# Kernel optimization log

Hardware: AMD Instinct MI355X
Metric: run time of the kernel (lower is better)

Reference implementation:

```python
import jax, jax.numpy as jnp
import numpy as np

B, N, C = 2, 384, 11            # images, proposals/img, classes (incl background)
RCN = 5                          # (xc, yc, w, h, angle_deg)
WEIGHTS = (10.0, 10.0, 5.0, 5.0, 1.0)
SCORE_THRESH = 0.05
NMS_THRESH = 0.5
DET_PER_IMG = 100
BBOX_XFORM_CLIP = float(np.log(1000.0 / 16.0))
EPS = 1e-8


def setup_inputs() -> dict:
    key = jax.random.key(0)
    k1, k2, k3, k4, k5 = jax.random.split(key, 5)
    class_logits = jax.random.normal(k1, (B * N, C), jnp.float32) * 2.0
    box_regression = jax.random.normal(k2, (B * N, C * RCN), jnp.float32) * 0.5
    xy = jax.random.uniform(k3, (B * N, 2), jnp.float32, 0.0, 1024.0)
    wh = jax.random.uniform(k4, (B * N, 2), jnp.float32, 16.0, 256.0)
    ang = jax.random.uniform(k5, (B * N, 1), jnp.float32, -90.0, 90.0)
    rrects = jnp.concatenate([xy, wh, ang], -1)
    return {"class_logits": class_logits, "box_regression": box_regression, "rrects": rrects}


def cross2(a, b):
    return a[..., 0] * b[..., 1] - a[..., 1] * b[..., 0]


def decode(rel, anchors):
    # rel (...,5) deltas, anchors (...,5) rotated boxes; relative angle coder
    wx, wy, ww, wh, wa = WEIGHTS
    dx = rel[..., 0] / wx
    dy = rel[..., 1] / wy
    dw = jnp.clip(rel[..., 2] / ww, None, BBOX_XFORM_CLIP)
    dh = jnp.clip(rel[..., 3] / wh, None, BBOX_XFORM_CLIP)
    da = rel[..., 4] / wa
    xc, yc, w, h, a = (anchors[..., i] for i in range(5))
    px = dx * w + xc
    py = dy * h + yc
    pw = jnp.exp(dw) * w
    ph = jnp.exp(dh) * h
    pa = da * (180.0 / np.pi) + a
    pa = (pa + 180.0) % 360.0 - 180.0
    return jnp.stack([px, py, pw, ph, pa], -1)


def corners(b):
    # (...,5) -> (...,4,2) rectangle corners (CCW in box frame)
    xc, yc, w, h, a = (b[..., i] for i in range(5))
    t = a * (np.pi / 180.0)
    c, s = jnp.cos(t), jnp.sin(t)
    hx, hy = w * 0.5, h * 0.5
    lx = jnp.stack([-hx, hx, hx, -hx], -1)
    ly = jnp.stack([-hy, -hy, hy, hy], -1)
    px = xc[..., None] + lx * c[..., None] - ly * s[..., None]
    py = yc[..., None] + lx * s[..., None] + ly * c[..., None]
    return jnp.stack([px, py], -1)


def inter_area(ca, cb):
    # intersection area of two convex quads (4,2),(4,2): candidate points =
    # 16 edge-edge intersections + 8 contained corners, sorted by angle, shoelace
    a0, b0 = ca, cb
    d1 = jnp.roll(ca, -1, 0) - ca
    d2 = jnp.roll(cb, -1, 0) - cb
    den = cross2(d1[:, None, :], d2[None, :, :])                # (4,4)
    diff = b0[None, :, :] - a0[:, None, :]
    den_s = jnp.where(jnp.abs(den) < EPS, 1.0, den)
    t = cross2(diff, d2[None, :, :]) / den_s
    u = cross2(diff, d1[:, None, :]) / den_s
    ok = (jnp.abs(den) >= EPS) & (t >= 0) & (t <= 1) & (u >= 0) & (u <= 1)
    pint = a0[:, None, :] + t[..., None] * d1[:, None, :]       # (4,4,2)

    def inside(p, cs):
        ev = jnp.roll(cs, -1, 0) - cs
        cr = cross2(ev[None, :, :], p[:, None, :] - cs[None, :, :])  # (4,4)
        return jnp.all(cr >= -1e-6, -1) | jnp.all(cr <= 1e-6, -1)

    pts = jnp.concatenate([pint.reshape(16, 2), ca, cb], 0)     # (24,2)
    msk = jnp.concatenate([ok.reshape(16), inside(ca, cb), inside(cb, ca)], 0)
    nv = jnp.sum(msk)
    cen = jnp.sum(pts * msk[:, None], 0) / jnp.maximum(nv, 1)
    pts = jnp.where(msk[:, None], pts, cen)                     # park invalid at centroid
    ang = jnp.arctan2(pts[:, 1] - cen[1], pts[:, 0] - cen[0])
    p = pts[jnp.argsort(ang)]
    area = 0.5 * jnp.abs(jnp.sum(cross2(p, jnp.roll(p, -1, 0))))
    return jnp.where(nv >= 3, area, 0.0)


def rotated_iou_matrix(boxes):
    # boxes (N,5) -> (N,N) rotated IoU
    cs = corners(boxes)
    area = boxes[:, 2] * boxes[:, 3]
    inter = jax.vmap(lambda ci: jax.vmap(lambda cj: inter_area(ci, cj))(cs))(cs)
    return inter / (area[:, None] + area[None, :] - inter + EPS)


def greedy_nms(iou, scores, valid):
    n = iou.shape[0]
    order = jnp.argsort(-jnp.where(valid, scores, -jnp.inf))
    ios = iou[order][:, order]
    vs = valid[order]
    idx = jnp.arange(n)

    def body(i, sup):
        cur_ok = (~sup[i]) & vs[i]
        return sup | (cur_ok & (ios[i] > NMS_THRESH) & (idx > i))

    sup = jax.lax.fori_loop(0, n, body, jnp.zeros((n,), bool))
    keep_sorted = (~sup) & vs
    return jnp.zeros((n,), bool).at[order].set(keep_sorted)


def reference(class_logits, box_regression, rrects):
    prob = jax.nn.softmax(class_logits, -1)                     # (M,C)
    rel = box_regression.reshape(B * N, C, RCN)
    dec = decode(rel, rrects[:, None, :])                       # (M,C,5)
    boxes = dec.reshape(B, N, C, RCN)
    scores = prob.reshape(B, N, C)
    fg_boxes = jnp.moveaxis(boxes[:, :, 1:, :], 2, 1)           # (B,C-1,N,5)
    fg_scores = jnp.moveaxis(scores[:, :, 1:], 2, 1)            # (B,C-1,N)
    valid = fg_scores > SCORE_THRESH
    iou = jax.vmap(jax.vmap(rotated_iou_matrix))(fg_boxes)      # (B,C-1,N,N)
    keep = jax.vmap(jax.vmap(greedy_nms))(iou, fg_scores, valid)
    flat_scores = jnp.where(keep, fg_scores, -1.0).reshape(B, (C - 1) * N)
    top_s, top_i = jax.lax.top_k(flat_scores, DET_PER_IMG)
    sel_boxes = jnp.take_along_axis(fg_boxes.reshape(B, (C - 1) * N, RCN), top_i[:, :, None], axis=1)
    labels = top_i // N + 1
    ok = top_s > 0.0
    out = jnp.concatenate([jnp.where(ok[..., None], sel_boxes, 0.0), jnp.where(ok, top_s, 0.0)[..., None]], -1)
    labels = jnp.where(ok, labels, 0)
    return out, labels
```

## Files before the change

kernel.cpp:

```cpp
#include <hip/hip_runtime.h>
#include <cmath>

#define NPROP 384
#define NB 2
#define NCLS 11
#define NFG 10
#define BC_TOTAL (NB*NFG)
#define M_TOTAL (NB*NPROP)
#define FLAT_PER_IMG (NFG*NPROP)
#define DET 100
#define PAIR_SLICE 3072

#define OFF_BOXES 0
#define OFF_AREA  38400
#define OFF_SCORE 46080
#define OFF_SUP   53760
#define OFF_KIDX  145920
#define OFF_KSC   153600
#define OFF_KCNT  161280
#define OFF_PCNT  161312
#define OFF_PAIRS 161344

typedef unsigned long long ull;

__device__ __forceinline__ void mk_corners(float px, float py, float pw, float ph, float pa,
                                           float cxo[4], float cyo[4]) {
    float t = pa * 0.017453292519943295f;
    float ct = cosf(t), st = sinf(t);
    float hx = pw*0.5f, hy = ph*0.5f;
    float lx[4] = {-hx, hx, hx, -hx};
    float ly[4] = {-hy, -hy, hy, hy};
#pragma unroll
    for (int k = 0; k < 4; ++k) {
        cxo[k] = px + lx[k]*ct - ly[k]*st;
        cyo[k] = py + lx[k]*st + ly[k]*ct;
    }
}

__device__ float inter_area_net(const float ax[4], const float ay[4],
                                const float bx[4], const float by[4]) {
    float d1x[4], d1y[4], d2x[4], d2y[4];
#pragma unroll
    for (int k = 0; k < 4; ++k) {
        int k1 = (k + 1) & 3;
        d1x[k] = ax[k1] - ax[k]; d1y[k] = ay[k1] - ay[k];
        d2x[k] = bx[k1] - bx[k]; d2y[k] = by[k1] - by[k];
    }
    float ex[32], ey[32];
    bool msk[24];
#pragma unroll
    for (int i = 0; i < 4; ++i) {
#pragma unroll
        for (int j = 0; j < 4; ++j) {
            float den = d1x[i]*d2y[j] - d1y[i]*d2x[j];
            float dfx = bx[j]-ax[i], dfy = by[j]-ay[i];
            float dens = (fabsf(den) < 1e-8f) ? 1.0f : den;
            float t = (dfx*d2y[j] - dfy*d2x[j]) / dens;
            float u = (dfx*d1y[i] - dfy*d1x[i]) / dens;
            bool ok = (fabsf(den) >= 1e-8f) && t >= 0.0f && t <= 1.0f
                                            && u >= 0.0f && u <= 1.0f;
            ex[i*4+j] = ax[i] + t*d1x[i];
            ey[i*4+j] = ay[i] + t*d1y[i];
            msk[i*4+j] = ok;
        }
    }
#pragma unroll
    for (int i = 0; i < 4; ++i) {
        bool allp = true, alln = true;
#pragma unroll
        for (int j = 0; j < 4; ++j) {
            float cr = d2x[j]*(ay[i]-by[j]) - d2y[j]*(ax[i]-bx[j]);
            allp = allp && (cr >= -1e-6f);
            alln = alln && (cr <= 1e-6f);
        }
        ex[16+i] = ax[i]; ey[16+i] = ay[i]; msk[16+i] = allp || alln;
    }
#pragma unroll
    for (int i = 0; i < 4; ++i) {
        bool allp = true, alln = true;
#pragma unroll
        for (int j = 0; j < 4; ++j) {
            float cr = d1x[j]*(by[i]-ay[j]) - d1y[j]*(bx[i]-ax[j]);
            allp = allp && (cr >= -1e-6f);
            alln = alln && (cr <= 1e-6f);
        }
        ex[20+i] = bx[i]; ey[20+i] = by[i]; msk[20+i] = allp || alln;
    }
    int nv = 0; float sx = 0.f, sy = 0.f;
#pragma unroll
    for (int k = 0; k < 24; ++k)
        if (msk[k]) { nv++; sx += ex[k]; sy += ey[k]; }
    float fm = (float)(nv > 1 ? nv : 1);
    float cx = sx / fm, cy = sy / fm;
    unsigned key[32];
#pragma unroll
    for (int k = 0; k < 24; ++k) {
        float qx = msk[k] ? ex[k] : cx;
        float qy = msk[k] ? ey[k] : cy;
        ex[k] = qx; ey[k] = qy;
        float dx = qx - cx, dy = qy - cy;
        float den = fabsf(dx) + fabsf(dy);
        float r = (den > 0.0f) ? dy / den : 0.0f;
        float p = (dx >= 0.0f) ? r : ((dy >= 0.0f) ? 2.0f - r : -2.0f - r);
        p = p + 0.0f;
        unsigned u = __float_as_uint(p);
        u = (u & 0x80000000u) ? ~u : (u | 0x80000000u);
        key[k] = (u & 0xFFFFFFE0u) | (unsigned)k;
    }
#pragma unroll
    for (int k = 24; k < 32; ++k) { key[k] = 0xFFFFFFFFu; ex[k] = 0.f; ey[k] = 0.f; }
#pragma unroll
    for (int k = 2; k <= 32; k <<= 1) {
#pragma unroll
        for (int j = k >> 1; j > 0; j >>= 1) {
#pragma unroll
            for (int i = 0; i < 32; ++i) {
                int l = i ^ j;
                if (l > i) {
                    bool up = ((i & k) == 0);
                    unsigned ka = key[i], kb = key[l];
                    bool sw = up ? (ka > kb) : (ka < kb);
                    float xa = ex[i], xb = ex[l];
                    float ya = ey[i], yb = ey[l];
                    key[i] = sw ? kb : ka; key[l] = sw ? ka : kb;
                    ex[i]  = sw ? xb : xa; ex[l]  = sw ? xa : xb;
                    ey[i]  = sw ? yb : ya; ey[l]  = sw ? ya : yb;
                }
            }
        }
    }
    float s = 0.f;
#pragma unroll
    for (int k = 0; k < 24; ++k) {
        int n = (k + 1 == 24) ? 0 : (k + 1);
        s += ex[k]*ey[n] - ey[k]*ex[n];
    }
    float area = 0.5f * fabsf(s);
    return (nv >= 3) ? area : 0.0f;
}

__device__ __forceinline__ void eval_pair_glob(float* ws, int bc, int hi, int lo) {
    const float* boxes = ws + OFF_BOXES;
    const float* areaA = ws + OFF_AREA;
    unsigned int* supw = (unsigned int*)(ws + OFF_SUP);
    int rowi = bc*NPROP + hi, rowj = bc*NPROP + lo;
    float axp[4], ayp[4], bxp[4], byp[4];
    mk_corners(boxes[rowi*5+0], boxes[rowi*5+1], boxes[rowi*5+2],
               boxes[rowi*5+3], boxes[rowi*5+4], axp, ayp);
    mk_corners(boxes[rowj*5+0], boxes[rowj*5+1], boxes[rowj*5+2],
               boxes[rowj*5+3], boxes[rowj*5+4], bxp, byp);
    float inter = inter_area_net(axp, ayp, bxp, byp);
    float iou = inter / (areaA[rowi] + areaA[rowj] - inter + 1e-8f);
    if (iou > 0.5f)
        atomicOr(&supw[rowi*12 + (lo >> 5)], 1u << (lo & 31));
}

__global__ __launch_bounds__(384)
void pairgen_kernel(const float* __restrict__ logits,
                    const float* __restrict__ boxreg,
                    const float* __restrict__ rrects,
                    float* __restrict__ ws,
                    float* __restrict__ out) {
    __shared__ float pxL[NPROP], pyL[NPROP], radL[NPROP], areaL[NPROP], scoreL[NPROP];
    __shared__ int   origL[NPROP];
    __shared__ int   wbase[8];
    __shared__ int   pcntS;
    int bc = blockIdx.x, t = threadIdx.x;
    int b = bc / NFG, cls = (bc % NFG) + 1;
    int wv = t >> 6, lane = t & 63;

    int gq = bc*NPROP + t;
    if (gq < NB*DET*6 + NB*DET) out[gq] = 0.0f;
    if (t == 0) pcntS = 0;
    {
        unsigned int* supw = (unsigned int*)(ws + OFF_SUP) + bc*NPROP*12;
        for (int k = t; k < NPROP*12; k += NPROP) supw[k] = 0u;
    }
    float prob;
    {
        int m = b*NPROP + t;
        float lg[NCLS];
        float mx = -INFINITY;
#pragma unroll
        for (int c = 0; c < NCLS; ++c) { lg[c] = logits[m*NCLS+c]; mx = fmaxf(mx, lg[c]); }
        float sum = 0.f;
#pragma unroll
        for (int c = 0; c < NCLS; ++c) sum += expf(lg[c]-mx);
        prob = expf(lg[cls]-mx) / sum;
        float axc = rrects[m*5+0], ayc = rrects[m*5+1];
        float aw  = rrects[m*5+2], ah  = rrects[m*5+3], aa = rrects[m*5+4];
        const float* rel = boxreg + m*(NCLS*5) + cls*5;
        float dx = rel[0] / 10.0f;
        float dy = rel[1] / 10.0f;
        float dw = fminf(rel[2] / 5.0f, 4.1351665567423205f);
        float dh = fminf(rel[3] / 5.0f, 4.1351665567423205f);
        float da = rel[4];
        float px = dx*aw + axc;
        float py = dy*ah + ayc;
        float pw = expf(dw)*aw;
        float ph = expf(dh)*ah;
        float pa = da*57.29577951308232f + aa;
        float xm = pa + 180.0f;
        float r = fmodf(xm, 360.0f);
        if (r < 0.0f) r += 360.0f;
        pa = r - 180.0f;
        pxL[t]=px; pyL[t]=py; areaL[t]=pw*ph; scoreL[t]=prob;
        radL[t]=0.5f*sqrtf(pw*pw + ph*ph);
        float* boxes = ws + OFF_BOXES;
        int o = bc*NPROP + t;
        boxes[o*5+0]=px; boxes[o*5+1]=py; boxes[o*5+2]=pw; boxes[o*5+3]=ph; boxes[o*5+4]=pa;
        ws[OFF_AREA + o]  = pw*ph;
        ws[OFF_SCORE + o] = prob;
    }
    bool vi = prob > 0.05f;
    ull vb = __ballot(vi);
    if (lane == 0) wbase[wv] = __popcll(vb);
    __syncthreads();
    if (t == 0) {
        int s = 0;
#pragma unroll
        for (int w = 0; w < 6; ++w) { int c = wbase[w]; wbase[w] = s; s += c; }
        wbase[6] = s;
    }
    __syncthreads();
    if (vi) origL[wbase[wv] + (int)__popcll(vb & ((1ull << lane) - 1ull))] = t;
    __syncthreads();
    int cnt = wbase[6];

    unsigned int* pairs = (unsigned int*)(ws + OFF_PAIRS) + bc*PAIR_SLICE;
    for (int a = wv; a < cnt; a += 6) {
        int ia = origL[a];
        float cxa = pxL[ia], cya = pyL[ia], ra = radL[ia], Aa = areaL[ia], sa = scoreL[ia];
        for (int b0 = a + 1; b0 < cnt; b0 += 64) {
            int bb = b0 + lane;
            bool go = false; int ib = 0;
            if (bb < cnt) {
                ib = origL[bb];
                float ddx = cxa - pxL[ib], ddy = cya - pyL[ib];
                float rr = ra + radL[ib];
                go = (ddx*ddx + ddy*ddy <= rr*rr);
                float Ab = areaL[ib];
                float mn = fminf(Aa, Ab);
                go = go && (3.0f*mn > Aa + Ab);
            }
            ull m = __ballot(go);
            int base = 0;
            if (lane == 0 && m) base = atomicAdd(&pcntS, __popcll(m));
            base = __shfl(base, 0);
            if (go) {
                float sb = scoreL[ib];
                bool afirst = (sa > sb) || (sa == sb && ia < ib);
                int hi = afirst ? ia : ib;
                int lo = afirst ? ib : ia;
                int pos = base + (int)__popcll(m & ((1ull << lane) - 1ull));
                if (pos < PAIR_SLICE)
                    pairs[pos] = ((unsigned)hi << 10) | (unsigned)lo;
                else
                    eval_pair_glob(ws, bc, hi, lo);
            }
        }
    }
    __syncthreads();
    if (t == 0) ((unsigned int*)(ws + OFF_PCNT))[bc] = (unsigned)pcntS;
}

__global__ __launch_bounds__(256)
void heavy_kernel(float* __restrict__ ws) {
    int bc = blockIdx.x >> 4;
    int chunk = blockIdx.x & 15;
    unsigned n = ((const unsigned int*)(ws + OFF_PCNT))[bc];
    if (n > PAIR_SLICE) n = PAIR_SLICE;
    const unsigned int* pairs = (const unsigned int*)(ws + OFF_PAIRS) + bc*PAIR_SLICE;
    for (unsigned p = chunk*256u + threadIdx.x; p < n; p += 4096u) {
        unsigned pk = pairs[p];
        eval_pair_glob(ws, bc, (int)(pk >> 10), (int)(pk & 0x3FFu));
    }
}

__global__ __launch_bounds__(384)
void nms_kernel(float* __restrict__ ws) {
    __shared__ ull keyL[NPROP];
    __shared__ int orderL[NPROP];
    __shared__ ull supL[NPROP*6];
    __shared__ unsigned char keepS[NPROP];
    __shared__ int wcntS[8];
    int bc = blockIdx.x, t = threadIdx.x;
    int wv = t >> 6, lane = t & 63;
    const float* scoreA = ws + OFF_SCORE;
    const ull* supG = (const ull*)(ws + OFF_SUP);
    float sc = scoreA[bc*NPROP + t];
    bool vi = sc > 0.05f;
    ull myk = vi ? (((ull)__float_as_uint(sc) << 32) | (ull)(0xFFFFFFFFu - (unsigned)t))
                 : (ull)(0xFFFFFFFFu - (unsigned)t);
    keyL[t] = myk;
    keepS[t] = 0;
    ull vb = __ballot(vi);
    if (lane == 0) wcntS[wv] = __popcll(vb);
    __syncthreads();
    {
        int r = 0;
        for (int k = 0; k < NPROP; k += 8) {
            int acc = 0;
#pragma unroll
            for (int q = 0; q < 8; ++q) acc += (keyL[k+q] > myk) ? 1 : 0;
            r += acc;
        }
        orderL[r] = t;
    }
    for (int k = t; k < NPROP*6; k += NPROP) supL[k] = supG[bc*NPROP*6 + k];
    __syncthreads();
    int NV = wcntS[0] + wcntS[1] + wcntS[2] + wcntS[3] + wcntS[4] + wcntS[5];
    if (t < 64) {
        int ord0 = orderL[lane],      ord1 = orderL[64+lane];
        int ord2 = orderL[128+lane],  ord3 = orderL[192+lane];
        int ord4 = orderL[256+lane],  ord5 = orderL[320+lane];
        ull mask = 0ull;
        int o_cur = __shfl(ord0, 0);
        ull row_cur = (lane < 6) ? supL[o_cur*6 + lane] : 0ull;
        for (int p = 0; p < NV; ++p) {
            int pn = (p + 1 < NPROP) ? (p + 1) : 0;
            int seg = pn >> 6, sl = pn & 63;
            int on = __shfl(ord0, sl);
            on = (seg == 1) ? __shfl(ord1, sl) : on;
            on = (seg == 2) ? __shfl(ord2, sl) : on;
            on = (seg == 3) ? __shfl(ord3, sl) : on;
            on = (seg == 4) ? __shfl(ord4, sl) : on;
            on = (seg == 5) ? __shfl(ord5, sl) : on;
            ull row_next = (lane < 6) ? supL[on*6 + lane] : 0ull;
            bool myhit = (lane == (o_cur >> 6)) && ((mask >> (o_cur & 63)) & 1ull);
            ull bal = __ballot(myhit);
            if (bal == 0ull) {
                if (lane == 0) keepS[o_cur] = 1;
                mask |= row_cur;
            }
            row_cur = row_next;
            o_cur = on;
        }
    }
    __syncthreads();
    bool kp = keepS[t] != 0;
    ull bal = __ballot(kp);
    if (lane == 0) wcntS[wv] = __popcll(bal);
    __syncthreads();
    if (t == 0) {
        int s = 0;
#pragma unroll
        for (int w = 0; w < 6; ++w) { int c = wcntS[w]; wcntS[w] = s; s += c; }
        ((unsigned int*)(ws + OFF_KCNT))[bc] = (unsigned)s;
    }
    __syncthreads();
    if (kp) {
        int pos = wcntS[wv] + (int)__popcll(bal & ((1ull << lane) - 1ull));
        ((unsigned int*)(ws + OFF_KIDX))[bc*NPROP + pos] = (unsigned)((bc % NFG)*NPROP + t);
        (ws + OFF_KSC)[bc*NPROP + pos] = sc;
    }
}

__global__ __launch_bounds__(256)
void topk_kernel(const float* __restrict__ ws, float* __restrict__ out) {
    __shared__ ull keyL[FLAT_PER_IMG];
    int b = blockIdx.x >> 4;
    int slice = blockIdx.x & 15;
    int t = threadIdx.x;
    const unsigned int* kidx2 = (const unsigned int*)(ws + OFF_KIDX);
    const float* ksc2 = ws + OFF_KSC;
    const unsigned int* kcnt2 = (const unsigned int*)(ws + OFF_KCNT);
    const float* boxes = ws + OFF_BOXES;
    int offs[NFG], cnts[NFG];
    int K = 0;
#pragma unroll
    for (int fg = 0; fg < NFG; ++fg) {
        cnts[fg] = (int)kcnt2[b*NFG + fg];
        offs[fg] = K;
        K += cnts[fg];
    }
#pragma unroll
    for (int fg = 0; fg < NFG; ++fg) {
        int bc = b*NFG + fg;
        for (int k = t; k < cnts[fg]; k += 256) {
            unsigned sb = __float_as_uint(ksc2[bc*NPROP + k]);
            unsigned f  = kidx2[bc*NPROP + k];
            keyL[offs[fg] + k] = ((ull)sb << 32) | (ull)(0xFFFFFFFFu - f);
        }
    }
    int KP = (K + 15) & ~15;
    for (int k = K + t; k < KP; k += 256) keyL[k] = 0ull;
    __syncthreads();
    int e = slice*256 + t;
    if (e >= K) return;
    ull my = keyL[e];
    int r = 0;
    for (int k = 0; k < KP; k += 16) {
        int acc = 0;
#pragma unroll
        for (int q = 0; q < 16; ++q)
            acc += (keyL[k+q] > my) ? 1 : 0;
        r += acc;
    }
    if (r < DET) {
        unsigned f = 0xFFFFFFFFu - (unsigned)(my & 0xFFFFFFFFu);
        float s = __uint_as_float((unsigned)(my >> 32));
        int src = b*FLAT_PER_IMG + (int)f;
        float* row = out + (b*DET + r)*6;
#pragma unroll
        for (int q = 0; q < 5; ++q) row[q] = boxes[src*5+q];
        row[5] = s;
        out[NB*DET*6 + b*DET + r] = (float)(f / NPROP + 1);
    }
}

extern "C" void kernel_launch(void* const* d_in, const int* in_sizes, int n_in,
                              void* d_out, int out_size, void* d_ws, size_t ws_size,
                              hipStream_t stream) {
    const float* logits = (const float*)d_in[0];
    const float* boxreg = (const float*)d_in[1];
    const float* rrects = (const float*)d_in[2];
    float* out = (float*)d_out;
    float* ws  = (float*)d_ws;
    (void)in_sizes; (void)n_in; (void)out_size; (void)ws_size;

    pairgen_kernel<<<BC_TOTAL, NPROP, 0, stream>>>(logits, boxreg, rrects, ws, out);
    heavy_kernel<<<BC_TOTAL * 16, 256, 0, stream>>>(ws);
    nms_kernel<<<BC_TOTAL, NPROP, 0, stream>>>(ws);
    topk_kernel<<<NB * 16, 256, 0, stream>>>(ws, out);
}
```

Before: 143.2 us.

## Fuse four NMS stages into one cooperative kernel with grid syncs

Merges the pair-generation, pair-evaluation, NMS and top-k kernels into a single cooperative launch of 160 blocks of 384 threads, separated by grid-wide syncs. Each stage reuses one shared memory buffer. The aim is to remove three kernel launch gaps and their inter-kernel overhead. In exchange it pays grid.sync costs, and the heavy stage and top-k are repartitioned: 8 chunks per class instead of 16, and 10 slices of 384 per image.

After: 191.7 us. 33.9% more time.

```diff
diff --git a/kernel.cpp b/kernel.cpp
--- a/kernel.cpp
+++ b/kernel.cpp
@@ -1,5 +1,8 @@
 #include <hip/hip_runtime.h>
+#include <hip/hip_cooperative_groups.h>
 #include <cmath>
+
+namespace cg = cooperative_groups;
 
 #define NPROP 384
 #define NB 2
@@ -10,6 +13,7 @@
 #define FLAT_PER_IMG (NFG*NPROP)
 #define DET 100
 #define PAIR_SLICE 3072
+#define GRID_BLKS 160
 
 #define OFF_BOXES 0
 #define OFF_AREA  38400
@@ -155,257 +159,265 @@
         atomicOr(&supw[rowi*12 + (lo >> 5)], 1u << (lo & 31));
 }
 
+#define SMEM_BYTES 30720
+
 __global__ __launch_bounds__(384)
-void pairgen_kernel(const float* __restrict__ logits,
-                    const float* __restrict__ boxreg,
-                    const float* __restrict__ rrects,
-                    float* __restrict__ ws,
-                    float* __restrict__ out) {
-    __shared__ float pxL[NPROP], pyL[NPROP], radL[NPROP], areaL[NPROP], scoreL[NPROP];
-    __shared__ int   origL[NPROP];
-    __shared__ int   wbase[8];
-    __shared__ int   pcntS;
-    int bc = blockIdx.x, t = threadIdx.x;
-    int b = bc / NFG, cls = (bc % NFG) + 1;
+void fused_kernel(const float* __restrict__ logits,
+                  const float* __restrict__ boxreg,
+                  const float* __restrict__ rrects,
+                  float* __restrict__ ws,
+                  float* __restrict__ out) {
+    cg::grid_group grid = cg::this_grid();
+    __shared__ __align__(16) unsigned char smemRaw[SMEM_BYTES];
+    __shared__ int auxA[8];
+    __shared__ int auxB;
+    int blk = blockIdx.x, t = threadIdx.x;
     int wv = t >> 6, lane = t & 63;
 
-    int gq = bc*NPROP + t;
-    if (gq < NB*DET*6 + NB*DET) out[gq] = 0.0f;
-    if (t == 0) pcntS = 0;
+    if (blk < BC_TOTAL) {
+        float* pxL    = (float*)smemRaw;
+        float* pyL    = pxL + NPROP;
+        float* radL   = pyL + NPROP;
+        float* areaL  = radL + NPROP;
+        float* scoreL = areaL + NPROP;
+        int*   origL  = (int*)(scoreL + NPROP);
+        int bc = blk;
+        int b = bc / NFG, cls = (bc % NFG) + 1;
+        int gq = bc*NPROP + t;
+        if (gq < NB*DET*6 + NB*DET) out[gq] = 0.0f;
+        if (t == 0) auxB = 0;
+        {
+            unsigned int* supw = (unsigned int*)(ws + OFF_SUP) + bc*NPROP*12;
+            for (int k = t; k < NPROP*12; k += NPROP) supw[k] = 0u;
+        }
+        float prob;
+        {
+            int m = b*NPROP + t;
+            float lg[NCLS];
+            float mx = -INFINITY;
+#pragma unroll
+            for (int c = 0; c < NCLS; ++c) { lg[c] = logits[m*NCLS+c]; mx = fmaxf(mx, lg[c]); }
+            float sum = 0.f;
+#pragma unroll
+            for (int c = 0; c < NCLS; ++c) sum += expf(lg[c]-mx);
+            prob = expf(lg[cls]-mx) / sum;
+            float axc = rrects[m*5+0], ayc = rrects[m*5+1];
+            float aw  = rrects[m*5+2], ah  = rrects[m*5+3], aa = rrects[m*5+4];
+            const float* rel = boxreg + m*(NCLS*5) + cls*5;
+            float dx = rel[0] / 10.0f;
+            float dy = rel[1] / 10.0f;
+            float dw = fminf(rel[2] / 5.0f, 4.1351665567423205f);
+            float dh = fminf(rel[3] / 5.0f, 4.1351665567423205f);
+            float da = rel[4];
+            float px = dx*aw + axc;
+            float py = dy*ah + ayc;
+            float pw = expf(dw)*aw;
+            float ph = expf(dh)*ah;
+            float pa = da*57.29577951308232f + aa;
+            float xm = pa + 180.0f;
+            float r = fmodf(xm, 360.0f);
+            if (r < 0.0f) r += 360.0f;
+            pa = r - 180.0f;
+            pxL[t]=px; pyL[t]=py; areaL[t]=pw*ph; scoreL[t]=prob;
+            radL[t]=0.5f*sqrtf(pw*pw + ph*ph);
+            float* boxes = ws + OFF_BOXES;
+            int o = bc*NPROP + t;
+            boxes[o*5+0]=px; boxes[o*5+1]=py; boxes[o*5+2]=pw; boxes[o*5+3]=ph; boxes[o*5+4]=pa;
+            ws[OFF_AREA + o]  = pw*ph;
+            ws[OFF_SCORE + o] = prob;
+        }
+        bool vi = prob > 0.05f;
+        ull vb = __ballot(vi);
+        if (lane == 0) auxA[wv] = __popcll(vb);
+        __syncthreads();
+        if (t == 0) {
+            int s = 0;
+#pragma unroll
+            for (int w = 0; w < 6; ++w) { int c = auxA[w]; auxA[w] = s; s += c; }
+            auxA[6] = s;
+        }
+        __syncthreads();
+        if (vi) origL[auxA[wv] + (int)__popcll(vb & ((1ull << lane) - 1ull))] = t;
+        __syncthreads();
+        int cnt = auxA[6];
+        unsigned int* pairs = (unsigned int*)(ws + OFF_PAIRS) + bc*PAIR_SLICE;
+        for (int a = wv; a < cnt; a += 6) {
+            int ia = origL[a];
+            float cxa = pxL[ia], cya = pyL[ia], ra = radL[ia], Aa = areaL[ia], sa = scoreL[ia];
+            for (int b0 = a + 1; b0 < cnt; b0 += 64) {
+                int bb = b0 + lane;
+                bool go = false; int ib = 0;
+                if (bb < cnt) {
+                    ib = origL[bb];
+                    float ddx = cxa - pxL[ib], ddy = cya - pyL[ib];
+                    float rr = ra + radL[ib];
+                    go = (ddx*ddx + ddy*ddy <= rr*rr);
+                    float Ab = areaL[ib];
+                    float mn = fminf(Aa, Ab);
+                    go = go && (3.0f*mn > Aa + Ab);
+                }
+                ull m = __ballot(go);
+                int base = 0;
+                if (lane == 0 && m) base = atomicAdd(&auxB, __popcll(m));
+                base = __shfl(base, 0);
+                if (go) {
+                    float sb = scoreL[ib];
+                    bool afirst = (sa > sb) || (sa == sb && ia < ib);
+                    int hi = afirst ? ia : ib;
+                    int lo = afirst ? ib : ia;
+                    int pos = base + (int)__popcll(m & ((1ull << lane) - 1ull));
+                    if (pos < PAIR_SLICE)
+                        pairs[pos] = ((unsigned)hi << 10) | (unsigned)lo;
+                    else
+                        eval_pair_glob(ws, bc, hi, lo);
+                }
+            }
+        }
+        __syncthreads();
+        if (t == 0) ((unsigned int*)(ws + OFF_PCNT))[bc] = (unsigned)auxB;
+    }
+    grid.sync();
+
     {
-        unsigned int* supw = (unsigned int*)(ws + OFF_SUP) + bc*NPROP*12;
-        for (int k = t; k < NPROP*12; k += NPROP) supw[k] = 0u;
-    }
-    float prob;
-    {
-        int m = b*NPROP + t;
-        float lg[NCLS];
-        float mx = -INFINITY;
-#pragma unroll
-        for (int c = 0; c < NCLS; ++c) { lg[c] = logits[m*NCLS+c]; mx = fmaxf(mx, lg[c]); }
-        float sum = 0.f;
-#pragma unroll
-        for (int c = 0; c < NCLS; ++c) sum += expf(lg[c]-mx);
-        prob = expf(lg[cls]-mx) / sum;
-        float axc = rrects[m*5+0], ayc = rrects[m*5+1];
-        float aw  = rrects[m*5+2], ah  = rrects[m*5+3], aa = rrects[m*5+4];
-        const float* rel = boxreg + m*(NCLS*5) + cls*5;
-        float dx = rel[0] / 10.0f;
-        float dy = rel[1] / 10.0f;
-        float dw = fminf(rel[2] / 5.0f, 4.1351665567423205f);
-        float dh = fminf(rel[3] / 5.0f, 4.1351665567423205f);
-        float da = rel[4];
-        float px = dx*aw + axc;
-        float py = dy*ah + ayc;
-        float pw = expf(dw)*aw;
-        float ph = expf(dh)*ah;
-        float pa = da*57.29577951308232f + aa;
-        float xm = pa + 180.0f;
-        float r = fmodf(xm, 360.0f);
-        if (r < 0.0f) r += 360.0f;
-        pa = r - 180.0f;
-        pxL[t]=px; pyL[t]=py; areaL[t]=pw*ph; scoreL[t]=prob;
-        radL[t]=0.5f*sqrtf(pw*pw + ph*ph);
-        float* boxes = ws + OFF_BOXES;
-        int o = bc*NPROP + t;
-        boxes[o*5+0]=px; boxes[o*5+1]=py; boxes[o*5+2]=pw; boxes[o*5+3]=ph; boxes[o*5+4]=pa;
-        ws[OFF_AREA + o]  = pw*ph;
-        ws[OFF_SCORE + o] = prob;
-    }
-    bool vi = prob > 0.05f;
-    ull vb = __ballot(vi);
-    if (lane == 0) wbase[wv] = __popcll(vb);
-    __syncthreads();
-    if (t == 0) {
-        int s = 0;
-#pragma unroll
-        for (int w = 0; w < 6; ++w) { int c = wbase[w]; wbase[w] = s; s += c; }
-        wbase[6] = s;
-    }
-    __syncthreads();
-    if (vi) origL[wbase[wv] + (int)__popcll(vb & ((1ull << lane) - 1ull))] = t;
-    __syncthreads();
-    int cnt = wbase[6];
-
-    unsigned int* pairs = (unsigned int*)(ws + OFF_PAIRS) + bc*PAIR_SLICE;
-    for (int a = wv; a < cnt; a += 6) {
-        int ia = origL[a];
-        float cxa = pxL[ia], cya = pyL[ia], ra = radL[ia], Aa = areaL[ia], sa = scoreL[ia];
-        for (int b0 = a + 1; b0 < cnt; b0 += 64) {
-            int bb = b0 + lane;
-            bool go = false; int ib = 0;
-            if (bb < cnt) {
-                ib = origL[bb];
-                float ddx = cxa - pxL[ib], ddy = cya - pyL[ib];
-                float rr = ra + radL[ib];
-                go = (ddx*ddx + ddy*ddy <= rr*rr);
-                float Ab = areaL[ib];
-                float mn = fminf(Aa, Ab);
-                go = go && (3.0f*mn > Aa + Ab);
-            }
-            ull m = __ballot(go);
-            int base = 0;
-            if (lane == 0 && m) base = atomicAdd(&pcntS, __popcll(m));
-            base = __shfl(base, 0);
-            if (go) {
-                float sb = scoreL[ib];
-                bool afirst = (sa > sb) || (sa == sb && ia < ib);
-                int hi = afirst ? ia : ib;
-                int lo = afirst ? ib : ia;
-                int pos = base + (int)__popcll(m & ((1ull << lane) - 1ull));
-                if (pos < PAIR_SLICE)
-                    pairs[pos] = ((unsigned)hi << 10) | (unsigned)lo;
-                else
-                    eval_pair_glob(ws, bc, hi, lo);
-            }
-        }
-    }
-    __syncthreads();
-    if (t == 0) ((unsigned int*)(ws + OFF_PCNT))[bc] = (unsigned)pcntS;
-}
-
-__global__ __launch_bounds__(256)
-void heavy_kernel(float* __restrict__ ws) {
-    int bc = blockIdx.x >> 4;
-    int chunk = blockIdx.x & 15;
-    unsigned n = ((const unsigned int*)(ws + OFF_PCNT))[bc];
-    if (n > PAIR_SLICE) n = PAIR_SLICE;
-    const unsigned int* pairs = (const unsigned int*)(ws + OFF_PAIRS) + bc*PAIR_SLICE;
-    for (unsigned p = chunk*256u + threadIdx.x; p < n; p += 4096u) {
-        unsigned pk = pairs[p];
-        eval_pair_glob(ws, bc, (int)(pk >> 10), (int)(pk & 0x3FFu));
-    }
-}
-
-__global__ __launch_bounds__(384)
-void nms_kernel(float* __restrict__ ws) {
-    __shared__ ull keyL[NPROP];
-    __shared__ int orderL[NPROP];
-    __shared__ ull supL[NPROP*6];
-    __shared__ unsigned char keepS[NPROP];
-    __shared__ int wcntS[8];
-    int bc = blockIdx.x, t = threadIdx.x;
-    int wv = t >> 6, lane = t & 63;
-    const float* scoreA = ws + OFF_SCORE;
-    const ull* supG = (const ull*)(ws + OFF_SUP);
-    float sc = scoreA[bc*NPROP + t];
-    bool vi = sc > 0.05f;
-    ull myk = vi ? (((ull)__float_as_uint(sc) << 32) | (ull)(0xFFFFFFFFu - (unsigned)t))
-                 : (ull)(0xFFFFFFFFu - (unsigned)t);
-    keyL[t] = myk;
-    keepS[t] = 0;
-    ull vb = __ballot(vi);
-    if (lane == 0) wcntS[wv] = __popcll(vb);
-    __syncthreads();
-    {
-        int r = 0;
-        for (int k = 0; k < NPROP; k += 8) {
-            int acc = 0;
-#pragma unroll
-            for (int q = 0; q < 8; ++q) acc += (keyL[k+q] > myk) ? 1 : 0;
-            r += acc;
-        }
-        orderL[r] = t;
-    }
-    for (int k = t; k < NPROP*6; k += NPROP) supL[k] = supG[bc*NPROP*6 + k];
-    __syncthreads();
-    int NV = wcntS[0] + wcntS[1] + wcntS[2] + wcntS[3] + wcntS[4] + wcntS[5];
-    if (t < 64) {
-        int ord0 = orderL[lane],      ord1 = orderL[64+lane];
-        int ord2 = orderL[128+lane],  ord3 = orderL[192+lane];
-        int ord4 = orderL[256+lane],  ord5 = orderL[320+lane];
-        ull mask = 0ull;
-        int o_cur = __shfl(ord0, 0);
-        ull row_cur = (lane < 6) ? supL[o_cur*6 + lane] : 0ull;
-        for (int p = 0; p < NV; ++p) {
-            int pn = (p + 1 < NPROP) ? (p + 1) : 0;
-            int seg = pn >> 6, sl = pn & 63;
-            int on = __shfl(ord0, sl);
-            on = (seg == 1) ? __shfl(ord1, sl) : on;
-            on = (seg == 2) ? __shfl(ord2, sl) : on;
-            on = (seg == 3) ? __shfl(ord3, sl) : on;
-            on = (seg == 4) ? __shfl(ord4, sl) : on;
-            on = (seg == 5) ? __shfl(ord5, sl) : on;
-            ull row_next = (lane < 6) ? supL[on*6 + lane] : 0ull;
-            bool myhit = (lane == (o_cur >> 6)) && ((mask >> (o_cur & 63)) & 1ull);
-            ull bal = __ballot(myhit);
-            if (bal == 0ull) {
-                if (lane == 0) keepS[o_cur] = 1;
-                mask |= row_cur;
-            }
-            row_cur = row_next;
-            o_cur = on;
-        }
-    }
-    __syncthreads();
-    bool kp = keepS[t] != 0;
-    ull bal = __ballot(kp);
-    if (lane == 0) wcntS[wv] = __popcll(bal);
-    __syncthreads();
-    if (t == 0) {
-        int s = 0;
-#pragma unroll
-        for (int w = 0; w < 6; ++w) { int c = wcntS[w]; wcntS[w] = s; s += c; }
-        ((unsigned int*)(ws + OFF_KCNT))[bc] = (unsigned)s;
-    }
-    __syncthreads();
-    if (kp) {
-        int pos = wcntS[wv] + (int)__popcll(bal & ((1ull << lane) - 1ull));
-        ((unsigned int*)(ws + OFF_KIDX))[bc*NPROP + pos] = (unsigned)((bc % NFG)*NPROP + t);
-        (ws + OFF_KSC)[bc*NPROP + pos] = sc;
-    }
-}
-
-__global__ __launch_bounds__(256)
-void topk_kernel(const float* __restrict__ ws, float* __restrict__ out) {
-    __shared__ ull keyL[FLAT_PER_IMG];
-    int b = blockIdx.x >> 4;
-    int slice = blockIdx.x & 15;
-    int t = threadIdx.x;
-    const unsigned int* kidx2 = (const unsigned int*)(ws + OFF_KIDX);
-    const float* ksc2 = ws + OFF_KSC;
-    const unsigned int* kcnt2 = (const unsigned int*)(ws + OFF_KCNT);
-    const float* boxes = ws + OFF_BOXES;
-    int offs[NFG], cnts[NFG];
-    int K = 0;
-#pragma unroll
-    for (int fg = 0; fg < NFG; ++fg) {
-        cnts[fg] = (int)kcnt2[b*NFG + fg];
-        offs[fg] = K;
-        K += cnts[fg];
-    }
-#pragma unroll
-    for (int fg = 0; fg < NFG; ++fg) {
-        int bc = b*NFG + fg;
-        for (int k = t; k < cnts[fg]; k += 256) {
-            unsigned sb = __float_as_uint(ksc2[bc*NPROP + k]);
-            unsigned f  = kidx2[bc*NPROP + k];
-            keyL[offs[fg] + k] = ((ull)sb << 32) | (ull)(0xFFFFFFFFu - f);
-        }
-    }
-    int KP = (K + 15) & ~15;
-    for (int k = K + t; k < KP; k += 256) keyL[k] = 0ull;
-    __syncthreads();
-    int e = slice*256 + t;
-    if (e >= K) return;
-    ull my = keyL[e];
-    int r = 0;
-    for (int k = 0; k < KP; k += 16) {
-        int acc = 0;
-#pragma unroll
-        for (int q = 0; q < 16; ++q)
-            acc += (keyL[k+q] > my) ? 1 : 0;
-        r += acc;
-    }
-    if (r < DET) {
-        unsigned f = 0xFFFFFFFFu - (unsigned)(my & 0xFFFFFFFFu);
-        float s = __uint_as_float((unsigned)(my >> 32));
-        int src = b*FLAT_PER_IMG + (int)f;
-        float* row = out + (b*DET + r)*6;
-#pragma unroll
-        for (int q = 0; q < 5; ++q) row[q] = boxes[src*5+q];
-        row[5] = s;
-        out[NB*DET*6 + b*DET + r] = (float)(f / NPROP + 1);
+        int bc = blk >> 3;
+        int chunk = blk & 7;
+        unsigned n = ((const unsigned int*)(ws + OFF_PCNT))[bc];
+        if (n > PAIR_SLICE) n = PAIR_SLICE;
+        const unsigned int* pairs = (const unsigned int*)(ws + OFF_PAIRS) + bc*PAIR_SLICE;
+        for (unsigned p = chunk*384u + t; p < n; p += 8u*384u) {
+            unsigned pk = pairs[p];
+            eval_pair_glob(ws, bc, (int)(pk >> 10), (int)(pk & 0x3FFu));
+        }
+    }
+    grid.sync();
+
+    if (blk < BC_TOTAL) {
+        ull* keyL   = (ull*)smemRaw;
+        ull* supL   = (ull*)(smemRaw + 3072);
+        int* orderL = (int*)(smemRaw + 21504);
+        unsigned char* keepS = smemRaw + 23040;
+        int bc = blk;
+        const float* scoreA = ws + OFF_SCORE;
+        const ull* supG = (const ull*)(ws + OFF_SUP);
+        float sc = scoreA[bc*NPROP + t];
+        bool vi = sc > 0.05f;
+        ull myk = vi ? (((ull)__float_as_uint(sc) << 32) | (ull)(0xFFFFFFFFu - (unsigned)t))
+                     : (ull)(0xFFFFFFFFu - (unsigned)t);
+        keyL[t] = myk;
+        keepS[t] = 0;
+        ull vb = __ballot(vi);
+        if (lane == 0) auxA[wv] = __popcll(vb);
+        __syncthreads();
+        {
+            int r = 0;
+            for (int k = 0; k < NPROP; k += 8) {
+                int acc = 0;
+#pragma unroll
+                for (int q = 0; q < 8; ++q) acc += (keyL[k+q] > myk) ? 1 : 0;
+                r += acc;
+            }
+            orderL[r] = t;
+        }
+        for (int k = t; k < NPROP*6; k += NPROP) supL[k] = supG[bc*NPROP*6 + k];
+        __syncthreads();
+        int NV = auxA[0] + auxA[1] + auxA[2] + auxA[3] + auxA[4] + auxA[5];
+        if (t < 64) {
+            int ord0 = orderL[lane],      ord1 = orderL[64+lane];
+            int ord2 = orderL[128+lane],  ord3 = orderL[192+lane];
+            int ord4 = orderL[256+lane],  ord5 = orderL[320+lane];
+            ull mask = 0ull;
+            int o_cur = __shfl(ord0, 0);
+            ull row_cur = (lane < 6) ? supL[o_cur*6 + lane] : 0ull;
+            for (int p = 0; p < NV; ++p) {
+                int pn = (p + 1 < NPROP) ? (p + 1) : 0;
+                int seg = pn >> 6, sl = pn & 63;
+                int on = __shfl(ord0, sl);
+                on = (seg == 1) ? __shfl(ord1, sl) : on;
+                on = (seg == 2) ? __shfl(ord2, sl) : on;
+                on = (seg == 3) ? __shfl(ord3, sl) : on;
+                on = (seg == 4) ? __shfl(ord4, sl) : on;
+                on = (seg == 5) ? __shfl(ord5, sl) : on;
+                ull row_next = (lane < 6) ? supL[on*6 + lane] : 0ull;
+                bool myhit = (lane == (o_cur >> 6)) && ((mask >> (o_cur & 63)) & 1ull);
+                ull bal = __ballot(myhit);
+                if (bal == 0ull) {
+                    if (lane == 0) keepS[o_cur] = 1;
+                    mask |= row_cur;
+                }
+                row_cur = row_next;
+                o_cur = on;
+            }
+        }
+        __syncthreads();
+        bool kp = keepS[t] != 0;
+        ull bal = __ballot(kp);
+        if (lane == 0) auxA[wv] = __popcll(bal);
+        __syncthreads();
+        if (t == 0) {
+            int s = 0;
+#pragma unroll
+            for (int w = 0; w < 6; ++w) { int c = auxA[w]; auxA[w] = s; s += c; }
+            ((unsigned int*)(ws + OFF_KCNT))[bc] = (unsigned)s;
+        }
+        __syncthreads();
+        if (kp) {
+            int pos = auxA[wv] + (int)__popcll(bal & ((1ull << lane) - 1ull));
+            ((unsigned int*)(ws + OFF_KIDX))[bc*NPROP + pos] = (unsigned)((bc % NFG)*NPROP + t);
+            (ws + OFF_KSC)[bc*NPROP + pos] = sc;
+        }
+    }
+    grid.sync();
+
+    if (blk < 2*NFG) {
+        ull* keyT = (ull*)smemRaw;
+        int b = blk / NFG;
+        int slice = blk % NFG;
+        const unsigned int* kidx2 = (const unsigned int*)(ws + OFF_KIDX);
+        const float* ksc2 = ws + OFF_KSC;
+        const unsigned int* kcnt2 = (const unsigned int*)(ws + OFF_KCNT);
+        const float* boxes = ws + OFF_BOXES;
+        int offs[NFG], cnts[NFG];
+        int K = 0;
+#pragma unroll
+        for (int fg = 0; fg < NFG; ++fg) {
+            cnts[fg] = (int)kcnt2[b*NFG + fg];
+            offs[fg] = K;
+            K += cnts[fg];
+        }
+#pragma unroll
+        for (int fg = 0; fg < NFG; ++fg) {
+            int bc = b*NFG + fg;
+            for (int k = t; k < cnts[fg]; k += NPROP) {
+                unsigned sb = __float_as_uint(ksc2[bc*NPROP + k]);
+                unsigned f  = kidx2[bc*NPROP + k];
+                keyT[offs[fg] + k] = ((ull)sb << 32) | (ull)(0xFFFFFFFFu - f);
+            }
+        }
+        int KP = (K + 15) & ~15;
+        for (int k = K + t; k < KP; k += NPROP) keyT[k] = 0ull;
+        __syncthreads();
+        int e = slice*NPROP + t;
+        if (e < K) {
+            ull my = keyT[e];
+            int r = 0;
+            for (int k = 0; k < KP; k += 16) {
+                int acc = 0;
+#pragma unroll
+                for (int q = 0; q < 16; ++q)
+                    acc += (keyT[k+q] > my) ? 1 : 0;
+                r += acc;
+            }
+            if (r < DET) {
+                unsigned f = 0xFFFFFFFFu - (unsigned)(my & 0xFFFFFFFFu);
+                float s = __uint_as_float((unsigned)(my >> 32));
+                int src = b*FLAT_PER_IMG + (int)f;
+                float* row = out + (b*DET + r)*6;
+#pragma unroll
+                for (int q = 0; q < 5; ++q) row[q] = boxes[src*5+q];
+                row[5] = s;
+                out[NB*DET*6 + b*DET + r] = (float)(f / NPROP + 1);
+            }
+        }
     }
 }
 
@@ -419,8 +431,8 @@
     float* ws  = (float*)d_ws;
     (void)in_sizes; (void)n_in; (void)out_size; (void)ws_size;
 
-    pairgen_kernel<<<BC_TOTAL, NPROP, 0, stream>>>(logits, boxreg, rrects, ws, out);
-    heavy_kernel<<<BC_TOTAL * 16, 256, 0, stream>>>(ws);
-    nms_kernel<<<BC_TOTAL, NPROP, 0, stream>>>(ws);
-    topk_kernel<<<NB * 16, 256, 0, stream>>>(ws, out);
+    void* kargs[] = { (void*)&logits, (void*)&boxreg, (void*)&rrects,
+                      (void*)&ws, (void*)&out };
+    hipLaunchCooperativeKernel((void*)fused_kernel, dim3(GRID_BLKS), dim3(NPROP),
+                               kargs, 0, stream);
 }
```
